# Optimization experiments

Hardware: AMD Instinct MI355X
Metric: run time of the kernel (lower is better)

The kernel has to match this reference:

```python
import jax, jax.numpy as jnp
import numpy as np

D = 512
SCALE = 1.0 / np.sqrt(D).astype(np.float32)


def setup_inputs() -> dict:
    key = jax.random.key(0)
    ks = jax.random.split(key, 6)
    B, S = 8, 2048
    x = jax.random.normal(ks[0], (B, S, D), dtype=jnp.float32)
    bias = jax.random.normal(ks[1], (1,), dtype=jnp.float32)
    key_padding_mask = jax.random.randint(ks[2], (B, S), 0, 2).astype(jnp.bool_)
    # nn.Linear weights, stored as [out, in]; y = x @ W.T
    Wq = jax.random.normal(ks[3], (D, D), dtype=jnp.float32) * (1.0 / np.sqrt(D))
    Wk = jax.random.normal(ks[4], (D, D), dtype=jnp.float32) * (1.0 / np.sqrt(D))
    Wv = jax.random.normal(ks[5], (D, D), dtype=jnp.float32) * (1.0 / np.sqrt(D))
    return {"x": x, "bias": bias, "key_padding_mask": key_padding_mask,
            "Wq": Wq, "Wk": Wk, "Wv": Wv}


def reference(x, bias, key_padding_mask, Wq, Wk, Wv):
    # Projections (Linear without bias): [B,S,D] @ [D,D]^T
    Q = jnp.einsum('bsd,ed->bse', x, Wq)
    K = jnp.einsum('bsd,ed->bse', x, Wk)
    V = jnp.einsum('bsd,ed->bse', x, Wv)
    # Scaled scores with additive scalar bias: [B,S,S]
    scores = jnp.einsum('bqd,bkd->bqk', Q, K) * SCALE + bias
    # Key padding mask: mask keys (last dim) with -inf
    scores = jnp.where(key_padding_mask[:, None, :], -jnp.inf, scores)
    attn = jax.nn.softmax(scores, axis=-1)
    attn = jnp.nan_to_num(attn, nan=0.0)  # fully-masked rows -> 0
    # Dropout is inference no-op
    return jnp.einsum('bqk,bkd->bqd', attn, V)
```

## Files before the change

kernel.cpp:

```cpp
#include <hip/hip_runtime.h>

typedef short bf16x8 __attribute__((ext_vector_type(8)));
typedef float f32x4 __attribute__((ext_vector_type(4)));
typedef float f32x16 __attribute__((ext_vector_type(16)));

__device__ __forceinline__ ushort f2bf(float f) {
    union { float f; unsigned u; } v; v.f = f;
    unsigned r = (v.u + 0x7fffu + ((v.u >> 16) & 1u)) >> 16;
    return (ushort)r;
}
__device__ __forceinline__ float bf2f(ushort u) {
    union { unsigned u; float f; } v; v.u = ((unsigned)u) << 16;
    return v.f;
}
__device__ __forceinline__ void async_copy16(void* lds, const void* g) {
    __builtin_amdgcn_global_load_lds(
        (const __attribute__((address_space(1))) unsigned*)g,
        (__attribute__((address_space(3))) unsigned*)lds, 16, 0, 0);
}

__global__ __launch_bounds__(256)
void cvt_f32_bf16(const float* __restrict__ src, ushort* __restrict__ dst, int n) {
    int i = (blockIdx.x * 256 + threadIdx.x) * 4;
    if (i >= n) return;
    float4 v = *(const float4*)(src + i);
    ushort4 o;
    o.x = f2bf(v.x); o.y = f2bf(v.y); o.z = f2bf(v.z); o.w = f2bf(v.w);
    *(ushort4*)(dst + i) = o;
}

__global__ __launch_bounds__(256)
void cvt_wT(const float* __restrict__ in0, const float* __restrict__ in1,
            ushort* __restrict__ out0, ushort* __restrict__ out1)
{
    const float* in = blockIdx.z ? in1 : in0;
    ushort* out     = blockIdx.z ? out1 : out0;
    __shared__ ushort T[64][72];
    const int r0 = blockIdx.y * 64, c0 = blockIdx.x * 64;
    const int t = threadIdx.x;
    const int rr = t >> 3, cc8 = (t & 7) * 8;
    #pragma unroll
    for (int pass = 0; pass < 2; ++pass) {
        int r = rr + pass * 32;
        float4 a = *(const float4*)(in + (size_t)(r0 + r) * 512 + c0 + cc8);
        float4 bq = *(const float4*)(in + (size_t)(r0 + r) * 512 + c0 + cc8 + 4);
        T[r][cc8+0]=f2bf(a.x);  T[r][cc8+1]=f2bf(a.y);  T[r][cc8+2]=f2bf(a.z);  T[r][cc8+3]=f2bf(a.w);
        T[r][cc8+4]=f2bf(bq.x); T[r][cc8+5]=f2bf(bq.y); T[r][cc8+6]=f2bf(bq.z); T[r][cc8+7]=f2bf(bq.w);
    }
    __syncthreads();
    const int c = t >> 2, seg = (t & 3) * 16;
    ushort tmp[16];
    #pragma unroll
    for (int j = 0; j < 16; ++j) tmp[j] = T[seg + j][c];
    *(uint4*)(out + (size_t)(c0 + c) * 512 + r0 + seg)     = *(uint4*)&tmp[0];
    *(uint4*)(out + (size_t)(c0 + c) * 512 + r0 + seg + 8) = *(uint4*)&tmp[8];
}

__global__ __launch_bounds__(256)
void compact_mask(const int* __restrict__ mask, int* __restrict__ idx,
                  int* __restrict__ cnt)
{
    int seg = blockIdx.x, b = seg >> 1, half = seg & 1;
    const int* m = mask + b * 2048 + half * 1024;
    int t = threadIdx.x;
    __shared__ int sc[256];
    int v0 = (m[t*4+0] == 0), v1 = (m[t*4+1] == 0);
    int v2 = (m[t*4+2] == 0), v3 = (m[t*4+3] == 0);
    int c = v0 + v1 + v2 + v3;
    sc[t] = c; __syncthreads();
    for (int ofs = 1; ofs < 256; ofs <<= 1) {
        int x = (t >= ofs) ? sc[t - ofs] : 0;
        __syncthreads(); sc[t] += x; __syncthreads();
    }
    int pos = sc[t] - c + seg * 1024;
    if (v0) idx[pos++] = t*4+0;
    if (v1) idx[pos++] = t*4+1;
    if (v2) idx[pos++] = t*4+2;
    if (v3) idx[pos++] = t*4+3;
    if (t == 255) cnt[seg] = sc[255];
}

__global__ __launch_bounds__(256)
void gather_rows(const ushort* __restrict__ xb, const int* __restrict__ idx,
                 const int* __restrict__ cnt, ushort* __restrict__ xc)
{
    int seg = blockIdx.x, b = seg >> 1, half = seg & 1;
    int n = cnt[seg];
    int wave = threadIdx.x >> 6, lane = threadIdx.x & 63;
    int j0 = blockIdx.y * 64 + wave * 16;
    for (int i = 0; i < 16; ++i) {
        int j = j0 + i;
        uint4 val = {0u, 0u, 0u, 0u};
        if (j < n) {
            int src = idx[seg * 1024 + j];
            val = *(const uint4*)((const char*)xb +
                  ((size_t)(b * 2048 + half * 1024 + src)) * 1024 + lane * 16);
        }
        *(uint4*)((char*)xc + ((size_t)(seg * 1024 + j)) * 1024 + lane * 16) = val;
    }
}

__global__ __launch_bounds__(256, 2)
void gemm_bt(const ushort* __restrict__ A, const ushort* __restrict__ B,
             ushort* __restrict__ C, int M, int N, int K,
             const int* __restrict__ cntM, const int* __restrict__ cntN)
{
    const int mBase = blockIdx.y * 128, nBase = blockIdx.x * 128;
    if (cntM && (mBase & 1023) >= cntM[mBase >> 10]) return;
    if (cntN && (nBase & 1023) >= cntN[nBase >> 10]) return;

    __shared__ ushort As[128][32];
    __shared__ ushort Bs[128][32];
    const int tid = threadIdx.x;
    const int lane = tid & 63, wave = tid >> 6;
    const int wm = wave >> 1, wn = wave & 1;
    const int lr = lane & 15, lq = lane >> 4;
    const int sr = lane >> 2;
    const int sc = (lane & 3) * 8;

    f32x4 acc[4][4];
    #pragma unroll
    for (int i = 0; i < 4; ++i)
        #pragma unroll
        for (int j = 0; j < 4; ++j) acc[i][j] = (f32x4){0.f, 0.f, 0.f, 0.f};

    for (int k0 = 0; k0 < K; k0 += 32) {
        __syncthreads();
        #pragma unroll
        for (int j = 0; j < 2; ++j) {
            int rbase = wave * 32 + j * 16;
            async_copy16(&As[rbase][0], A + (size_t)(mBase + rbase + sr) * K + k0 + sc);
            async_copy16(&Bs[rbase][0], B + (size_t)(nBase + rbase + sr) * K + k0 + sc);
        }
        __syncthreads();
        bf16x8 af[4], bfr[4];
        #pragma unroll
        for (int mi = 0; mi < 4; ++mi) af[mi] = *(const bf16x8*)&As[wm * 64 + mi * 16 + lr][lq * 8];
        #pragma unroll
        for (int ni = 0; ni < 4; ++ni) bfr[ni] = *(const bf16x8*)&Bs[wn * 64 + ni * 16 + lr][lq * 8];
        #pragma unroll
        for (int mi = 0; mi < 4; ++mi)
            #pragma unroll
            for (int ni = 0; ni < 4; ++ni)
                acc[mi][ni] = __builtin_amdgcn_mfma_f32_16x16x32_bf16(af[mi], bfr[ni], acc[mi][ni], 0, 0, 0);
    }
    #pragma unroll
    for (int mi = 0; mi < 4; ++mi)
        #pragma unroll
        for (int ni = 0; ni < 4; ++ni)
            #pragma unroll
            for (int r = 0; r < 4; ++r) {
                int m = mBase + wm * 64 + mi * 16 + lq * 4 + r;
                int n = nBase + wn * 64 + ni * 16 + lr;
                C[(size_t)m * N + n] = f2bf(acc[mi][ni][r]);
            }
}

__global__ __launch_bounds__(256, 2)
void attn_kernel(const ushort* __restrict__ Qg, const ushort* __restrict__ Kcg,
                 const ushort* __restrict__ Vtcg, const int* __restrict__ cntg,
                 ushort* __restrict__ Pog, float* __restrict__ Mlg)
{
    const int S = 2048;
    const float SL2E = 0.0637587160f;

    __shared__ ushort Ks[32][548];
    __shared__ ushort Vs[512][36];
    __shared__ ushort Ps[2][32][36];

    const int b = blockIdx.y, qt = blockIdx.x, half = blockIdx.z;
    const int seg = b * 2 + half;
    const int tid = threadIdx.x, lane = tid & 63, wave = tid >> 6;
    const int lr = lane & 15, lq = lane >> 4;
    const int p = wave >> 1, s = wave & 1;
    const int l32 = lane & 31, lh = lane >> 5;

    const int n = cntg[seg];
    const int ntiles = (n + 31) >> 5;

    const ushort* Qp = Qg + ((size_t)b * S + qt * 64 + wave * 16 + lr) * 512;
    bf16x8 qf[16];
    #pragma unroll
    for (int c = 0; c < 16; ++c) qf[c] = *(const bf16x8*)(Qp + c * 32 + lq * 8);

    f32x16 o[8];
    #pragma unroll
    for (int i = 0; i < 8; ++i)
        #pragma unroll
        for (int r = 0; r < 16; ++r) o[i][r] = 0.f;
    float l_i[4] = {0.f, 0.f, 0.f, 0.f};

    const char* Kseg = (const char*)(Kcg + (size_t)seg * 1024 * 512);
    const char* Vseg = (const char*)Vtcg + (size_t)(seg * 1024) * 2;

    for (int kt = 0; kt < ntiles; ++kt) {
        const int key0 = kt * 32;
        __syncthreads();
        {
            const char* gK = Kseg + (size_t)key0 * 1024;
            #pragma unroll
            for (int i = 0; i < 8; ++i) {
                int row = wave * 8 + i;
                async_copy16(&Ks[row][0], gK + (size_t)row * 1024 + lane * 16);
            }
        }
        const bool va0 = (key0 + lr) < n;
        const bool va1 = (key0 + 16 + lr) < n;
        __syncthreads();
        uint4 vreg[8];
        {
            const char* gV = Vseg + (size_t)key0 * 2;
            #pragma unroll
            for (int i = 0; i < 8; ++i) {
                int off = i * 4096 + tid * 16;
                int row = off >> 6, col = off & 63;
                vreg[i] = *(const uint4*)(gV + (size_t)row * 32768 + col);
            }
        }
        f32x4 sf0 = (f32x4){0.f,0.f,0.f,0.f}, sf1 = (f32x4){0.f,0.f,0.f,0.f};
        #pragma unroll
        for (int ks = 0; ks < 16; ++ks) {
            bf16x8 kf0 = *(const bf16x8*)&Ks[lr][ks * 32 + lq * 8];
            bf16x8 kf1 = *(const bf16x8*)&Ks[16 + lr][ks * 32 + lq * 8];
            sf0 = __builtin_amdgcn_mfma_f32_16x16x32_bf16(qf[ks], kf0, sf0, 0, 0, 0);
            sf1 = __builtin_amdgcn_mfma_f32_16x16x32_bf16(qf[ks], kf1, sf1, 0, 0, 0);
        }
        #pragma unroll
        for (int r = 0; r < 4; ++r) {
            float p0 = va0 ? exp2f(fmaf(sf0[r], SL2E, -8.f)) : 0.f;
            float p1 = va1 ? exp2f(fmaf(sf1[r], SL2E, -8.f)) : 0.f;
            l_i[r] += p0 + p1;
            Ps[p][16 * s + lq * 4 + r][lr]      = f2bf(p0);
            Ps[p][16 * s + lq * 4 + r][16 + lr] = f2bf(p1);
        }
        #pragma unroll
        for (int i = 0; i < 8; ++i) {
            int off = i * 4096 + tid * 16;
            int row = off >> 6, col = off & 63;
            *(uint4*)((char*)Vs + row * 72 + col) = vreg[i];
        }
        __syncthreads();
        bf16x8 pA0 = *(const bf16x8*)&Ps[p][l32][lh * 8];
        bf16x8 pA1 = *(const bf16x8*)&Ps[p][l32][16 + lh * 8];
        #pragma unroll
        for (int dt = 0; dt < 8; ++dt) {
            int d = s * 256 + dt * 32 + l32;
            bf16x8 v0 = *(const bf16x8*)&Vs[d][lh * 8];
            bf16x8 v1 = *(const bf16x8*)&Vs[d][16 + lh * 8];
            o[dt] = __builtin_amdgcn_mfma_f32_32x32x16_bf16(pA0, v0, o[dt], 0, 0, 0);
            o[dt] = __builtin_amdgcn_mfma_f32_32x32x16_bf16(pA1, v1, o[dt], 0, 0, 0);
        }
    }
    #pragma unroll
    for (int r = 0; r < 4; ++r)
        #pragma unroll
        for (int off = 1; off < 16; off <<= 1)
            l_i[r] += __shfl_xor(l_i[r], off, 16);
    const size_t growbase = (size_t)half * 16384 + (size_t)b * S + qt * 64;
    if (lr == 0) {
        #pragma unroll
        for (int r = 0; r < 4; ++r)
            Mlg[growbase + wave * 16 + lq * 4 + r] = l_i[r];
    }
    ushort* Pop = Pog + (growbase + p * 32) * 512;
    #pragma unroll
    for (int dt = 0; dt < 8; ++dt) {
        int ocol = s * 256 + dt * 32 + l32;
        #pragma unroll
        for (int r = 0; r < 16; ++r) {
            int orow = (r & 3) + 8 * (r >> 2) + 4 * lh;
            Pop[(size_t)orow * 512 + ocol] = f2bf(o[dt][r]);
        }
    }
}

__global__ __launch_bounds__(256)
void combine_kernel(const ushort* __restrict__ Po, const float* __restrict__ Ml,
                    float* __restrict__ out)
{
    int i = (blockIdx.x * 256 + threadIdx.x) * 4;
    int row = i >> 9;
    float l = Ml[row] + Ml[16384 + row];
    float s = l > 0.f ? 1.f / l : 0.f;
    ushort4 p1 = *(const ushort4*)(Po + i);
    ushort4 p2 = *(const ushort4*)(Po + 8388608 + i);
    float4 o;
    o.x = (bf2f(p1.x) + bf2f(p2.x)) * s;
    o.y = (bf2f(p1.y) + bf2f(p2.y)) * s;
    o.z = (bf2f(p1.z) + bf2f(p2.z)) * s;
    o.w = (bf2f(p1.w) + bf2f(p2.w)) * s;
    *(float4*)(out + i) = o;
}

extern "C" void kernel_launch(void* const* d_in, const int* in_sizes, int n_in,
                              void* d_out, int out_size, void* d_ws, size_t ws_size,
                              hipStream_t stream) {
    const float* x  = (const float*)d_in[0];
    const int* mask = (const int*)d_in[2];
    const float* Wq = (const float*)d_in[3];
    const float* Wk = (const float*)d_in[4];
    const float* Wv = (const float*)d_in[5];
    float* out = (float*)d_out;

    ushort* ws   = (ushort*)d_ws;
    ushort* xb   = ws;
    ushort* wqT  = ws + 8388608;
    ushort* wkT  = wqT + 262144;
    ushort* wvb  = wkT + 262144;
    ushort* xc   = ws + 9175040;
    ushort* Pob  = ws + 9175040;
    ushort* Mb   = ws + 17563648;
    int*    idxb = (int*)(ws + 17825792);
    ushort* Kc   = ws + 25952256;
    ushort* Vtc  = ws + 34340864;
    float*  Mlb  = (float*)(ws + 42729472);
    int*    cntb = (int*)(ws + 42795008);

    cvt_f32_bf16<<<8192, 256, 0, stream>>>(x, xb, 8388608);
    cvt_f32_bf16<<<256, 256, 0, stream>>>(Wv, wvb, 262144);
    cvt_wT<<<dim3(8, 8, 2), 256, 0, stream>>>(Wq, Wk, wqT, wkT);
    compact_mask<<<16, 256, 0, stream>>>(mask, idxb, cntb);
    gather_rows<<<dim3(16, 16), 256, 0, stream>>>(xb, idxb, cntb, xc);
    gemm_bt<<<dim3(4, 4), 256, 0, stream>>>(wqT, wkT, Mb, 512, 512, 512, nullptr, nullptr);
    gemm_bt<<<dim3(4, 128), 256, 0, stream>>>(xc, Mb, Kc, 16384, 512, 512, cntb, nullptr);
    gemm_bt<<<dim3(128, 4), 256, 0, stream>>>(wvb, xc, Vtc, 512, 16384, 512, nullptr, cntb);
    attn_kernel<<<dim3(32, 8, 2), 256, 0, stream>>>(xb, Kc, Vtc, cntb, Pob, Mlb);
    combine_kernel<<<8192, 256, 0, stream>>>(Pob, Mlb, out);
}
```

Measured before the change: 242.3 us.

## Drop full x bf16 conversion, merge K/V GEMMs, prefetch K tiles in attention

```diff
diff --git a/kernel.cpp b/kernel.cpp
--- a/kernel.cpp
+++ b/kernel.cpp
@@ -18,6 +18,8 @@
         (const __attribute__((address_space(1))) unsigned*)g,
         (__attribute__((address_space(3))) unsigned*)lds, 16, 0, 0);
 }
+#define BAR_NONE() asm volatile("s_barrier" ::: "memory")
+#define BAR_LGKM() asm volatile("s_waitcnt lgkmcnt(0)\n\ts_barrier" ::: "memory")
 
 __global__ __launch_bounds__(256)
 void cvt_f32_bf16(const float* __restrict__ src, ushort* __restrict__ dst, int n) {
@@ -81,8 +83,8 @@
 }
 
 __global__ __launch_bounds__(256)
-void gather_rows(const ushort* __restrict__ xb, const int* __restrict__ idx,
-                 const int* __restrict__ cnt, ushort* __restrict__ xc)
+void gather_cvt(const float* __restrict__ x, const int* __restrict__ idx,
+                const int* __restrict__ cnt, ushort* __restrict__ xc)
 {
     int seg = blockIdx.x, b = seg >> 1, half = seg & 1;
     int n = cnt[seg];
@@ -93,22 +95,22 @@
         uint4 val = {0u, 0u, 0u, 0u};
         if (j < n) {
             int src = idx[seg * 1024 + j];
-            val = *(const uint4*)((const char*)xb +
-                  ((size_t)(b * 2048 + half * 1024 + src)) * 1024 + lane * 16);
-        }
-        *(uint4*)((char*)xc + ((size_t)(seg * 1024 + j)) * 1024 + lane * 16) = val;
-    }
-}
-
-__global__ __launch_bounds__(256, 2)
-void gemm_bt(const ushort* __restrict__ A, const ushort* __restrict__ B,
-             ushort* __restrict__ C, int M, int N, int K,
-             const int* __restrict__ cntM, const int* __restrict__ cntN)
-{
-    const int mBase = blockIdx.y * 128, nBase = blockIdx.x * 128;
-    if (cntM && (mBase & 1023) >= cntM[mBase >> 10]) return;
-    if (cntN && (nBase & 1023) >= cntN[nBase >> 10]) return;
-
+            const float* r = x + ((size_t)(b * 2048 + half * 1024 + src)) * 512 + lane * 8;
+            float4 a = *(const float4*)r, c4 = *(const float4*)(r + 4);
+            ushort tmp[8];
+            tmp[0]=f2bf(a.x); tmp[1]=f2bf(a.y); tmp[2]=f2bf(a.z); tmp[3]=f2bf(a.w);
+            tmp[4]=f2bf(c4.x); tmp[5]=f2bf(c4.y); tmp[6]=f2bf(c4.z); tmp[7]=f2bf(c4.w);
+            val = *(uint4*)tmp;
+        }
+        *(uint4*)(xc + ((size_t)(seg * 1024 + j)) * 512 + lane * 8) = val;
+    }
+}
+
+__device__ __forceinline__ void gemm_core(const ushort* __restrict__ A,
+                                          const ushort* __restrict__ B,
+                                          ushort* __restrict__ C,
+                                          int N, int K, int mBase, int nBase)
+{
     __shared__ ushort As[128][32];
     __shared__ ushort Bs[128][32];
     const int tid = threadIdx.x;
@@ -157,7 +159,31 @@
 }
 
 __global__ __launch_bounds__(256, 2)
-void attn_kernel(const ushort* __restrict__ Qg, const ushort* __restrict__ Kcg,
+void gemm_m(const ushort* __restrict__ A, const ushort* __restrict__ B,
+            ushort* __restrict__ C) {
+    gemm_core(A, B, C, 512, 512, blockIdx.y * 128, blockIdx.x * 128);
+}
+
+__global__ __launch_bounds__(256, 2)
+void gemm_kv(const ushort* __restrict__ xc, const ushort* __restrict__ Mb,
+             ushort* __restrict__ Kc, const ushort* __restrict__ wv,
+             ushort* __restrict__ Vtc, const int* __restrict__ cnt)
+{
+    const ushort *A, *B; ushort* C; int N, mBase, nBase;
+    if (blockIdx.z == 0) {
+        mBase = blockIdx.y * 128; nBase = blockIdx.x * 128;
+        if ((mBase & 1023) >= cnt[mBase >> 10]) return;
+        A = xc; B = Mb; C = Kc; N = 512;
+    } else {
+        mBase = blockIdx.x * 128; nBase = blockIdx.y * 128;
+        if ((nBase & 1023) >= cnt[nBase >> 10]) return;
+        A = wv; B = xc; C = Vtc; N = 16384;
+    }
+    gemm_core(A, B, C, N, 512, mBase, nBase);
+}
+
+__global__ __launch_bounds__(256, 2)
+void attn_kernel(const float* __restrict__ xg, const ushort* __restrict__ Kcg,
                  const ushort* __restrict__ Vtcg, const int* __restrict__ cntg,
                  ushort* __restrict__ Pog, float* __restrict__ Mlg)
 {
@@ -165,8 +191,8 @@
     const float SL2E = 0.0637587160f;
 
     __shared__ ushort Ks[32][548];
-    __shared__ ushort Vs[512][36];
-    __shared__ ushort Ps[2][32][36];
+    __shared__ ushort Vs[512][38];
+    __shared__ ushort Ps[2][32][38];
 
     const int b = blockIdx.y, qt = blockIdx.x, half = blockIdx.z;
     const int seg = b * 2 + half;
@@ -178,10 +204,19 @@
     const int n = cntg[seg];
     const int ntiles = (n + 31) >> 5;
 
-    const ushort* Qp = Qg + ((size_t)b * S + qt * 64 + wave * 16 + lr) * 512;
+    const float* Qp = xg + ((size_t)b * S + qt * 64 + wave * 16 + lr) * 512;
     bf16x8 qf[16];
     #pragma unroll
-    for (int c = 0; c < 16; ++c) qf[c] = *(const bf16x8*)(Qp + c * 32 + lq * 8);
+    for (int c = 0; c < 16; ++c) {
+        float4 a = *(const float4*)(Qp + c * 32 + lq * 8);
+        float4 d4 = *(const float4*)(Qp + c * 32 + lq * 8 + 4);
+        bf16x8 q;
+        q[0] = (short)f2bf(a.x);  q[1] = (short)f2bf(a.y);
+        q[2] = (short)f2bf(a.z);  q[3] = (short)f2bf(a.w);
+        q[4] = (short)f2bf(d4.x); q[5] = (short)f2bf(d4.y);
+        q[6] = (short)f2bf(d4.z); q[7] = (short)f2bf(d4.w);
+        qf[c] = q;
+    }
 
     f32x16 o[8];
     #pragma unroll
@@ -193,30 +228,32 @@
     const char* Kseg = (const char*)(Kcg + (size_t)seg * 1024 * 512);
     const char* Vseg = (const char*)Vtcg + (size_t)(seg * 1024) * 2;
 
+    uint4 xfer[8];
+    #pragma unroll
+    for (int i = 0; i < 8; ++i) {
+        int off = i * 4096 + tid * 16, row = off >> 10, col = off & 1023;
+        xfer[i] = *(const uint4*)(Kseg + (size_t)row * 1024 + col);
+    }
+
     for (int kt = 0; kt < ntiles; ++kt) {
         const int key0 = kt * 32;
-        __syncthreads();
-        {
-            const char* gK = Kseg + (size_t)key0 * 1024;
-            #pragma unroll
-            for (int i = 0; i < 8; ++i) {
-                int row = wave * 8 + i;
-                async_copy16(&Ks[row][0], gK + (size_t)row * 1024 + lane * 16);
-            }
-        }
-        const bool va0 = (key0 + lr) < n;
-        const bool va1 = (key0 + 16 + lr) < n;
-        __syncthreads();
-        uint4 vreg[8];
+        BAR_NONE();
+        #pragma unroll
+        for (int i = 0; i < 8; ++i) {
+            int off = i * 4096 + tid * 16, row = off >> 10, col = off & 1023;
+            *(uint4*)((char*)Ks + (size_t)row * 1096 + col) = xfer[i];
+        }
+        BAR_LGKM();
         {
             const char* gV = Vseg + (size_t)key0 * 2;
             #pragma unroll
             for (int i = 0; i < 8; ++i) {
-                int off = i * 4096 + tid * 16;
-                int row = off >> 6, col = off & 63;
-                vreg[i] = *(const uint4*)(gV + (size_t)row * 32768 + col);
+                int off = i * 4096 + tid * 16, row = off >> 6, col = off & 63;
+                xfer[i] = *(const uint4*)(gV + (size_t)row * 32768 + col);
             }
         }
+        const bool va0 = (key0 + lr) < n;
+        const bool va1 = (key0 + 16 + lr) < n;
         f32x4 sf0 = (f32x4){0.f,0.f,0.f,0.f}, sf1 = (f32x4){0.f,0.f,0.f,0.f};
         #pragma unroll
         for (int ks = 0; ks < 16; ++ks) {
@@ -235,13 +272,20 @@
         }
         #pragma unroll
         for (int i = 0; i < 8; ++i) {
-            int off = i * 4096 + tid * 16;
-            int row = off >> 6, col = off & 63;
-            *(uint4*)((char*)Vs + row * 72 + col) = vreg[i];
-        }
-        __syncthreads();
+            int off = i * 4096 + tid * 16, row = off >> 6, col = off & 63;
+            *(uint4*)((char*)Vs + (size_t)row * 76 + col) = xfer[i];
+        }
+        BAR_LGKM();
         bf16x8 pA0 = *(const bf16x8*)&Ps[p][l32][lh * 8];
         bf16x8 pA1 = *(const bf16x8*)&Ps[p][l32][16 + lh * 8];
+        if (kt + 1 < ntiles) {
+            const char* gK = Kseg + (size_t)(key0 + 32) * 1024;
+            #pragma unroll
+            for (int i = 0; i < 8; ++i) {
+                int off = i * 4096 + tid * 16, row = off >> 10, col = off & 1023;
+                xfer[i] = *(const uint4*)(gK + (size_t)row * 1024 + col);
+            }
+        }
         #pragma unroll
         for (int dt = 0; dt < 8; ++dt) {
             int d = s * 256 + dt * 32 + l32;
@@ -303,27 +347,24 @@
     float* out = (float*)d_out;
 
     ushort* ws   = (ushort*)d_ws;
-    ushort* xb   = ws;
-    ushort* wqT  = ws + 8388608;
+    ushort* Pob  = ws;
+    ushort* Mb   = ws;
+    int*    idxb = (int*)(ws + 262144);
+    ushort* wqT  = ws + 16777216;
     ushort* wkT  = wqT + 262144;
     ushort* wvb  = wkT + 262144;
-    ushort* xc   = ws + 9175040;
-    ushort* Pob  = ws + 9175040;
-    ushort* Mb   = ws + 17563648;
-    int*    idxb = (int*)(ws + 17825792);
+    ushort* xc   = ws + 17563648;
     ushort* Kc   = ws + 25952256;
     ushort* Vtc  = ws + 34340864;
     float*  Mlb  = (float*)(ws + 42729472);
     int*    cntb = (int*)(ws + 42795008);
 
-    cvt_f32_bf16<<<8192, 256, 0, stream>>>(x, xb, 8388608);
+    cvt_wT<<<dim3(8, 8, 2), 256, 0, stream>>>(Wq, Wk, wqT, wkT);
     cvt_f32_bf16<<<256, 256, 0, stream>>>(Wv, wvb, 262144);
-    cvt_wT<<<dim3(8, 8, 2), 256, 0, stream>>>(Wq, Wk, wqT, wkT);
     compact_mask<<<16, 256, 0, stream>>>(mask, idxb, cntb);
-    gather_rows<<<dim3(16, 16), 256, 0, stream>>>(xb, idxb, cntb, xc);
-    gemm_bt<<<dim3(4, 4), 256, 0, stream>>>(wqT, wkT, Mb, 512, 512, 512, nullptr, nullptr);
-    gemm_bt<<<dim3(4, 128), 256, 0, stream>>>(xc, Mb, Kc, 16384, 512, 512, cntb, nullptr);
-    gemm_bt<<<dim3(128, 4), 256, 0, stream>>>(wvb, xc, Vtc, 512, 16384, 512, nullptr, cntb);
-    attn_kernel<<<dim3(32, 8, 2), 256, 0, stream>>>(xb, Kc, Vtc, cntb, Pob, Mlb);
+    gather_cvt<<<dim3(16, 16), 256, 0, stream>>>(x, idxb, cntb, xc);
+    gemm_m<<<dim3(4, 4), 256, 0, stream>>>(wqT, wkT, Mb);
+    gemm_kv<<<dim3(4, 128, 2), 256, 0, stream>>>(xc, Mb, Kc, wvb, Vtc, cntb);
+    attn_kernel<<<dim3(32, 8, 2), 256, 0, stream>>>(x, Kc, Vtc, cntb, Pob, Mlb);
     combine_kernel<<<8192, 256, 0, stream>>>(Pob, Mlb, out);
 }
```

Result: slower. 410.7 us (+69.5%).

## Merge prep kernels into one launch and fuse K/V projection GEMMs

Applied to the files above, without the earlier changes.

```diff
diff --git a/kernel.cpp b/kernel.cpp
--- a/kernel.cpp
+++ b/kernel.cpp
@@ -20,69 +20,73 @@
 }
 
 __global__ __launch_bounds__(256)
-void cvt_f32_bf16(const float* __restrict__ src, ushort* __restrict__ dst, int n) {
-    int i = (blockIdx.x * 256 + threadIdx.x) * 4;
-    if (i >= n) return;
-    float4 v = *(const float4*)(src + i);
-    ushort4 o;
-    o.x = f2bf(v.x); o.y = f2bf(v.y); o.z = f2bf(v.z); o.w = f2bf(v.w);
-    *(ushort4*)(dst + i) = o;
+void prep_kernel(const float* __restrict__ x, const float* __restrict__ Wq,
+                 const float* __restrict__ Wk, const float* __restrict__ Wv,
+                 const int* __restrict__ mask,
+                 ushort* __restrict__ xb, ushort* __restrict__ wqT,
+                 ushort* __restrict__ wkT, ushort* __restrict__ wvb,
+                 int* __restrict__ idx, int* __restrict__ cnt)
+{
+    const int bid = blockIdx.x, t = threadIdx.x;
+    if (bid < 8192) {
+        int i = (bid * 256 + t) * 4;
+        float4 v = *(const float4*)(x + i);
+        ushort4 o;
+        o.x = f2bf(v.x); o.y = f2bf(v.y); o.z = f2bf(v.z); o.w = f2bf(v.w);
+        *(ushort4*)(xb + i) = o;
+    } else if (bid < 8320) {
+        __shared__ ushort T[64][72];
+        int r = bid - 8192;
+        const int z = r >> 6; r &= 63;
+        const float* in = z ? Wk : Wq;
+        ushort* out     = z ? wkT : wqT;
+        const int r0 = (r >> 3) * 64, c0 = (r & 7) * 64;
+        const int rr = t >> 3, cc8 = (t & 7) * 8;
+        #pragma unroll
+        for (int pass = 0; pass < 2; ++pass) {
+            int rw = rr + pass * 32;
+            float4 a = *(const float4*)(in + (size_t)(r0 + rw) * 512 + c0 + cc8);
+            float4 bq = *(const float4*)(in + (size_t)(r0 + rw) * 512 + c0 + cc8 + 4);
+            T[rw][cc8+0]=f2bf(a.x);  T[rw][cc8+1]=f2bf(a.y);  T[rw][cc8+2]=f2bf(a.z);  T[rw][cc8+3]=f2bf(a.w);
+            T[rw][cc8+4]=f2bf(bq.x); T[rw][cc8+5]=f2bf(bq.y); T[rw][cc8+6]=f2bf(bq.z); T[rw][cc8+7]=f2bf(bq.w);
+        }
+        __syncthreads();
+        const int c = t >> 2, seg = (t & 3) * 16;
+        ushort tmp[16];
+        #pragma unroll
+        for (int j = 0; j < 16; ++j) tmp[j] = T[seg + j][c];
+        *(uint4*)(out + (size_t)(c0 + c) * 512 + r0 + seg)     = *(uint4*)&tmp[0];
+        *(uint4*)(out + (size_t)(c0 + c) * 512 + r0 + seg + 8) = *(uint4*)&tmp[8];
+    } else if (bid < 8576) {
+        int i = ((bid - 8320) * 256 + t) * 4;
+        float4 v = *(const float4*)(Wv + i);
+        ushort4 o;
+        o.x = f2bf(v.x); o.y = f2bf(v.y); o.z = f2bf(v.z); o.w = f2bf(v.w);
+        *(ushort4*)(wvb + i) = o;
+    } else {
+        __shared__ int sc[256];
+        int seg = bid - 8576, b = seg >> 1, half = seg & 1;
+        const int* m = mask + b * 2048 + half * 1024;
+        int v0 = (m[t*4+0] == 0), v1 = (m[t*4+1] == 0);
+        int v2 = (m[t*4+2] == 0), v3 = (m[t*4+3] == 0);
+        int c = v0 + v1 + v2 + v3;
+        sc[t] = c; __syncthreads();
+        for (int ofs = 1; ofs < 256; ofs <<= 1) {
+            int xx = (t >= ofs) ? sc[t - ofs] : 0;
+            __syncthreads(); sc[t] += xx; __syncthreads();
+        }
+        int pos = sc[t] - c + seg * 1024;
+        if (v0) idx[pos++] = t*4+0;
+        if (v1) idx[pos++] = t*4+1;
+        if (v2) idx[pos++] = t*4+2;
+        if (v3) idx[pos++] = t*4+3;
+        if (t == 255) cnt[seg] = sc[255];
+    }
 }
 
 __global__ __launch_bounds__(256)
-void cvt_wT(const float* __restrict__ in0, const float* __restrict__ in1,
-            ushort* __restrict__ out0, ushort* __restrict__ out1)
-{
-    const float* in = blockIdx.z ? in1 : in0;
-    ushort* out     = blockIdx.z ? out1 : out0;
-    __shared__ ushort T[64][72];
-    const int r0 = blockIdx.y * 64, c0 = blockIdx.x * 64;
-    const int t = threadIdx.x;
-    const int rr = t >> 3, cc8 = (t & 7) * 8;
-    #pragma unroll
-    for (int pass = 0; pass < 2; ++pass) {
-        int r = rr + pass * 32;
-        float4 a = *(const float4*)(in + (size_t)(r0 + r) * 512 + c0 + cc8);
-        float4 bq = *(const float4*)(in + (size_t)(r0 + r) * 512 + c0 + cc8 + 4);
-        T[r][cc8+0]=f2bf(a.x);  T[r][cc8+1]=f2bf(a.y);  T[r][cc8+2]=f2bf(a.z);  T[r][cc8+3]=f2bf(a.w);
-        T[r][cc8+4]=f2bf(bq.x); T[r][cc8+5]=f2bf(bq.y); T[r][cc8+6]=f2bf(bq.z); T[r][cc8+7]=f2bf(bq.w);
-    }
-    __syncthreads();
-    const int c = t >> 2, seg = (t & 3) * 16;
-    ushort tmp[16];
-    #pragma unroll
-    for (int j = 0; j < 16; ++j) tmp[j] = T[seg + j][c];
-    *(uint4*)(out + (size_t)(c0 + c) * 512 + r0 + seg)     = *(uint4*)&tmp[0];
-    *(uint4*)(out + (size_t)(c0 + c) * 512 + r0 + seg + 8) = *(uint4*)&tmp[8];
-}
-
-__global__ __launch_bounds__(256)
-void compact_mask(const int* __restrict__ mask, int* __restrict__ idx,
-                  int* __restrict__ cnt)
-{
-    int seg = blockIdx.x, b = seg >> 1, half = seg & 1;
-    const int* m = mask + b * 2048 + half * 1024;
-    int t = threadIdx.x;
-    __shared__ int sc[256];
-    int v0 = (m[t*4+0] == 0), v1 = (m[t*4+1] == 0);
-    int v2 = (m[t*4+2] == 0), v3 = (m[t*4+3] == 0);
-    int c = v0 + v1 + v2 + v3;
-    sc[t] = c; __syncthreads();
-    for (int ofs = 1; ofs < 256; ofs <<= 1) {
-        int x = (t >= ofs) ? sc[t - ofs] : 0;
-        __syncthreads(); sc[t] += x; __syncthreads();
-    }
-    int pos = sc[t] - c + seg * 1024;
-    if (v0) idx[pos++] = t*4+0;
-    if (v1) idx[pos++] = t*4+1;
-    if (v2) idx[pos++] = t*4+2;
-    if (v3) idx[pos++] = t*4+3;
-    if (t == 255) cnt[seg] = sc[255];
-}
-
-__global__ __launch_bounds__(256)
-void gather_rows(const ushort* __restrict__ xb, const int* __restrict__ idx,
-                 const int* __restrict__ cnt, ushort* __restrict__ xc)
+void gather_cvt(const float* __restrict__ x, const int* __restrict__ idx,
+                const int* __restrict__ cnt, ushort* __restrict__ xc)
 {
     int seg = blockIdx.x, b = seg >> 1, half = seg & 1;
     int n = cnt[seg];
@@ -93,22 +97,22 @@
         uint4 val = {0u, 0u, 0u, 0u};
         if (j < n) {
             int src = idx[seg * 1024 + j];
-            val = *(const uint4*)((const char*)xb +
-                  ((size_t)(b * 2048 + half * 1024 + src)) * 1024 + lane * 16);
-        }
-        *(uint4*)((char*)xc + ((size_t)(seg * 1024 + j)) * 1024 + lane * 16) = val;
-    }
-}
-
-__global__ __launch_bounds__(256, 2)
-void gemm_bt(const ushort* __restrict__ A, const ushort* __restrict__ B,
-             ushort* __restrict__ C, int M, int N, int K,
-             const int* __restrict__ cntM, const int* __restrict__ cntN)
-{
-    const int mBase = blockIdx.y * 128, nBase = blockIdx.x * 128;
-    if (cntM && (mBase & 1023) >= cntM[mBase >> 10]) return;
-    if (cntN && (nBase & 1023) >= cntN[nBase >> 10]) return;
-
+            const float* r = x + ((size_t)(b * 2048 + half * 1024 + src)) * 512 + lane * 8;
+            float4 a = *(const float4*)r, c4 = *(const float4*)(r + 4);
+            ushort tmp[8];
+            tmp[0]=f2bf(a.x); tmp[1]=f2bf(a.y); tmp[2]=f2bf(a.z); tmp[3]=f2bf(a.w);
+            tmp[4]=f2bf(c4.x); tmp[5]=f2bf(c4.y); tmp[6]=f2bf(c4.z); tmp[7]=f2bf(c4.w);
+            val = *(uint4*)tmp;
+        }
+        *(uint4*)(xc + ((size_t)(seg * 1024 + j)) * 512 + lane * 8) = val;
+    }
+}
+
+__device__ __forceinline__ void gemm_core(const ushort* __restrict__ A,
+                                          const ushort* __restrict__ B,
+                                          ushort* __restrict__ C,
+                                          int N, int K, int mBase, int nBase)
+{
     __shared__ ushort As[128][32];
     __shared__ ushort Bs[128][32];
     const int tid = threadIdx.x;
@@ -154,6 +158,30 @@
                 int n = nBase + wn * 64 + ni * 16 + lr;
                 C[(size_t)m * N + n] = f2bf(acc[mi][ni][r]);
             }
+}
+
+__global__ __launch_bounds__(256, 2)
+void gemm_m(const ushort* __restrict__ A, const ushort* __restrict__ B,
+            ushort* __restrict__ C) {
+    gemm_core(A, B, C, 512, 512, blockIdx.y * 128, blockIdx.x * 128);
+}
+
+__global__ __launch_bounds__(256, 2)
+void gemm_kv(const ushort* __restrict__ xc, const ushort* __restrict__ Mb,
+             ushort* __restrict__ Kc, const ushort* __restrict__ wv,
+             ushort* __restrict__ Vtc, const int* __restrict__ cnt)
+{
+    const ushort *A, *B; ushort* C; int N, mBase, nBase;
+    if (blockIdx.z == 0) {
+        mBase = blockIdx.y * 128; nBase = blockIdx.x * 128;
+        if ((mBase & 1023) >= cnt[mBase >> 10]) return;
+        A = xc; B = Mb; C = Kc; N = 512;
+    } else {
+        mBase = blockIdx.x * 128; nBase = blockIdx.y * 128;
+        if ((nBase & 1023) >= cnt[nBase >> 10]) return;
+        A = wv; B = xc; C = Vtc; N = 16384;
+    }
+    gemm_core(A, B, C, N, 512, mBase, nBase);
 }
 
 __global__ __launch_bounds__(256, 2)
@@ -316,14 +344,11 @@
     float*  Mlb  = (float*)(ws + 42729472);
     int*    cntb = (int*)(ws + 42795008);
 
-    cvt_f32_bf16<<<8192, 256, 0, stream>>>(x, xb, 8388608);
-    cvt_f32_bf16<<<256, 256, 0, stream>>>(Wv, wvb, 262144);
-    cvt_wT<<<dim3(8, 8, 2), 256, 0, stream>>>(Wq, Wk, wqT, wkT);
-    compact_mask<<<16, 256, 0, stream>>>(mask, idxb, cntb);
-    gather_rows<<<dim3(16, 16), 256, 0, stream>>>(xb, idxb, cntb, xc);
-    gemm_bt<<<dim3(4, 4), 256, 0, stream>>>(wqT, wkT, Mb, 512, 512, 512, nullptr, nullptr);
-    gemm_bt<<<dim3(4, 128), 256, 0, stream>>>(xc, Mb, Kc, 16384, 512, 512, cntb, nullptr);
-    gemm_bt<<<dim3(128, 4), 256, 0, stream>>>(wvb, xc, Vtc, 512, 16384, 512, nullptr, cntb);
+    prep_kernel<<<8592, 256, 0, stream>>>(x, Wq, Wk, Wv, mask,
+                                          xb, wqT, wkT, wvb, idxb, cntb);
+    gather_cvt<<<dim3(16, 16), 256, 0, stream>>>(x, idxb, cntb, xc);
+    gemm_m<<<dim3(4, 4), 256, 0, stream>>>(wqT, wkT, Mb);
+    gemm_kv<<<dim3(4, 128, 2), 256, 0, stream>>>(xc, Mb, Kc, wvb, Vtc, cntb);
     attn_kernel<<<dim3(32, 8, 2), 256, 0, stream>>>(xb, Kc, Vtc, cntb, Pob, Mlb);
     combine_kernel<<<8192, 256, 0, stream>>>(Pob, Mlb, out);
 }
```

Measured after the change: 229.0 us. 1.06x faster.
